# Performance work log

Measured on AMD Instinct MI355X. Metric: run time of the kernel, lower is better.

## Reference

```python
import jax, jax.numpy as jnp
import numpy as np

# --- model hyperparameters (match init_kwargs / TrajectoryDecoder defaults) ---
R, T, KREG = 3, 16, 8          # num_radii, num_theta, reg_dim
RADIUS = 40.0                  # radius_scale
VEHICLE_HIDDEN = 16
MAP_HIDDEN = 8
IN_CH = VEHICLE_HIDDEN + MAP_HIDDEN  # 24
PREDICT_WINDOW = 30
TWO_PI = 2.0 * np.pi


def _reg_roll(f):
    # f: [..., C, k] -> [..., C, k(l), k(m)] with entry f[..., c, (m-l)%k]
    m = jnp.arange(KREG)[None, :]
    l = jnp.arange(KREG)[:, None]
    return f[..., (m - l) % KREG]


def _equilinear(W, f):
    # equivariant linear map between regular reps = circular (group) conv over reg dim
    # W: [out, in, k], f: [..., in, k] -> [..., out, k]
    return jnp.einsum('oil,...ilm->...om', W, _reg_roll(f))


def _reg2rho1(f, w):
    # frequency-1 Fourier projection of the regular rep -> rho1 (2-vector); 2 free params
    ang = TWO_PI * jnp.arange(KREG) / KREG
    c, s = jnp.cos(ang), jnp.sin(ang)
    W2 = jnp.stack([w[0] * c - w[1] * s, w[0] * s + w[1] * c], axis=-1)  # [k, 2]
    return jnp.einsum('...cm,md->...cd', f, W2)


def _cts_aggregate(dst_p, src_p, H, src_mask):
    # Continuous conv aggregation: bilinear interpolation of a polar-binned kernel
    # already contracted with source features.
    # H: [B, S, R, T, O, k] per-source, per-(radius,theta)-bin transformed features
    B, S, O = src_p.shape[0], src_p.shape[1], H.shape[-2]
    rel = src_p[:, None, :, :] - dst_p[:, :, None, :]      # [B, Nd, S, 2]
    d = jnp.sqrt(jnp.sum(rel * rel, axis=-1) + 1e-12)      # [B, Nd, S]
    valid = (d < RADIUS).astype(dst_p.dtype) * src_mask[:, None, :]
    win = jnp.maximum(1.0 - (d / RADIUS) ** 2, 0.0) ** 3   # CConv window
    cnt = jnp.maximum(jnp.sum(valid, axis=-1, keepdims=True), 1.0)
    base_w = valid * win / cnt
    # radial interpolation (clamped linear)
    u = jnp.clip(d / RADIUS, 0.0, 1.0) * (R - 1)
    r0f = jnp.floor(u); wr = u - r0f
    r0 = r0f.astype(jnp.int32); r1 = jnp.minimum(r0 + 1, R - 1)
    # angular interpolation (circular linear)
    t = ((jnp.arctan2(rel[..., 1], rel[..., 0]) / TWO_PI) % 1.0) * T
    t0f = jnp.floor(t); wt = t - t0f
    t0 = t0f.astype(jnp.int32) % T; t1 = (t0 + 1) % T
    Hf = H.reshape(B, S, R * T, O, KREG)
    bidx = jnp.arange(B)[:, None, None]
    sidx = jnp.arange(S)[None, None, :]
    out = jnp.zeros((B, dst_p.shape[1], O, KREG), dtype=dst_p.dtype)
    for ri, ti, cw in ((r0, t0, (1 - wr) * (1 - wt)),
                       (r0, t1, (1 - wr) * wt),
                       (r1, t0, wr * (1 - wt)),
                       (r1, t1, wr * wt)):
        g = Hf[bidx, sidx, ri * T + ti]                    # [B, Nd, S, O, k] irregular gather
        out = out + jnp.einsum('bns,bnsok->bnok', base_w * cw, g)
    return out


def _conv_reg(K, src_p, dst_p, f, src_mask):
    # EquiCtsConv2dRegToReg: per-bin group conv over reg dim, then continuous-conv gather
    H = jnp.einsum('rtoil,bsilm->bsrtom', K, _reg_roll(f))
    return _cts_aggregate(dst_p, src_p, H, src_mask)


def _conv_rho1(K, src_p, dst_p, v, src_mask):
    # EquiCtsConv2dRho1ToReg (in_channels=1): contract 2-vector input per bin
    H = jnp.einsum('rtomd,bsd->bsrtom', K, v)
    return _cts_aggregate(dst_p, src_p, H, src_mask)


def _decode(p, feat, car_mask, K_vehicle, Wd_vehicle, K_conv1, Wd1, K_conv2, Wd2):
    out = _conv_reg(K_vehicle, p, p, feat, car_mask) + _equilinear(Wd_vehicle, feat)
    for K, Wd in ((K_conv1, Wd1), (K_conv2, Wd2)):
        inf = jax.nn.relu(out)
        oc = _conv_reg(K, p, p, inf, car_mask)
        od = _equilinear(Wd, inf)
        out = oc + od + out if od.shape[-2] == out.shape[-2] else oc + od
    return jax.nn.relu(out)


def _forward(p, feat, map_p, map_feat, car_mask, map_mask,
             K_vehicle, Wd_vehicle, K_conv1, Wd1, K_conv2, Wd2,
             Wd_back, w_rho1, K_map):
    outputs = []
    output = _decode(p, feat, car_mask, K_vehicle, Wd_vehicle, K_conv1, Wd1, K_conv2, Wd2)
    delta = _reg2rho1(output, w_rho1)                      # [B, N, 3, 2]
    outputs.append(delta.at[..., 0, :].add(p))
    for _ in range(1, PREDICT_WINDOW):
        p = p + delta[..., 0, :]
        back = jnp.tanh(_equilinear(Wd_back, output))      # [B, N, 16, k]
        feat_v = feat[..., :VEHICLE_HIDDEN, :] * back
        enc = jax.nn.relu(_conv_rho1(K_map, map_p, p, map_feat, map_mask))  # MapEncoder
        feat = jnp.concatenate([feat_v, enc], axis=-2)     # [B, N, 24, k]
        output = _decode(p, feat, car_mask, K_vehicle, Wd_vehicle, K_conv1, Wd1, K_conv2, Wd2)
        delta = _reg2rho1(output, w_rho1)
        outputs.append(delta.at[..., 0, :].add(p))
    return jnp.stack(outputs, axis=0)                      # [30, B, N, 3, 2]


def setup_inputs() -> dict:
    key = jax.random.key(0)
    ks = jax.random.split(key, 13)
    B, N, M = 8, 64, 1024
    sc = 0.1
    return {
        'p': jax.random.normal(ks[0], (B, N, 2)) * 20.0,
        'feat': jax.random.normal(ks[1], (B, N, IN_CH, KREG)),
        'map_p': jax.random.normal(ks[2], (B, M, 2)) * 20.0,
        'map_feat': jax.random.normal(ks[3], (B, M, 2)),
        'car_mask': jnp.ones((B, N), dtype=jnp.float32),
        'map_mask': jnp.ones((B, M), dtype=jnp.float32),
        'K_vehicle': jax.random.normal(ks[4], (R, T, 8, IN_CH, KREG)) * sc,
        'Wd_vehicle': jax.random.normal(ks[5], (8, IN_CH, KREG)) * sc,
        'K_conv1': jax.random.normal(ks[6], (R, T, 8, 8, KREG)) * sc,
        'Wd1': jax.random.normal(ks[7], (8, 8, KREG)) * sc,
        'K_conv2': jax.random.normal(ks[8], (R, T, 3, 8, KREG)) * sc,
        'Wd2': jax.random.normal(ks[9], (3, 8, KREG)) * sc,
        'Wd_back': jax.random.normal(ks[10], (VEHICLE_HIDDEN, 3, KREG)) * sc,
        'w_rho1': jax.random.normal(ks[11], (2,)) * sc,
        'K_map': jax.random.normal(ks[12], (R, T, MAP_HIDDEN, KREG, 2)) * sc,
    }


def reference(p, feat, map_p, map_feat, car_mask, map_mask,
              K_vehicle, Wd_vehicle, K_conv1, Wd1, K_conv2, Wd2,
              Wd_back, w_rho1, K_map):
    return _forward(p, feat, map_p, map_feat, car_mask, map_mask,
                    K_vehicle, Wd_vehicle, K_conv1, Wd1, K_conv2, Wd2,
                    Wd_back, w_rho1, K_map)
```

## Files before the change

### kernel.cpp

```cpp
#include <hip/hip_runtime.h>
#include <math.h>

#define NB 8
#define NV 64
#define NM 1024
#define NR 3
#define NT 16
#define KR 8
#define RTOT 48
#define RADIUSF 40.0f
#define TWO_PIF 6.283185307179586f

__device__ __forceinline__ void pair_geom(float relx, float rely, float mask,
                                          float& valid, float& win,
                                          int bin[4], float cw[4]) {
    float d = sqrtf(relx * relx + rely * rely + 1e-12f);
    valid = (d < RADIUSF) ? mask : 0.0f;
    float q = d * (1.0f / RADIUSF);
    float w1 = fmaxf(1.0f - q * q, 0.0f);
    win = w1 * w1 * w1;
    float u = fminf(fmaxf(q, 0.0f), 1.0f) * (float)(NR - 1);
    float r0f = floorf(u);
    float wr = u - r0f;
    int r0 = (int)r0f;
    int r1 = min(r0 + 1, NR - 1);
    float a = atan2f(rely, relx) * (1.0f / TWO_PIF);
    a = a - floorf(a);
    float t = a * (float)NT;
    float t0f = floorf(t);
    float wt = t - t0f;
    int t0 = ((int)t0f) & (NT - 1);
    int t1 = (t0 + 1) & (NT - 1);
    bin[0] = r0 * NT + t0; cw[0] = (1.0f - wr) * (1.0f - wt);
    bin[1] = r0 * NT + t1; cw[1] = (1.0f - wr) * wt;
    bin[2] = r1 * NT + t0; cw[2] = wr * (1.0f - wt);
    bin[3] = r1 * NT + t1; cw[3] = wr * wt;
}

__global__ __launch_bounds__(256) void k_trans(
        const float* __restrict__ Kv, const float* __restrict__ K1g,
        const float* __restrict__ K2g, float4* __restrict__ KTv,
        float4* __restrict__ KT1, float4* __restrict__ KT2) {
    int idx = blockIdx.x * 256 + threadIdx.x;
    if (idx < 48 * 384) {
        int j = idx / 384, p = idx % 384;
        KTv[idx] = *(const float4*)(Kv + p * 192 + j * 4);
    } else if (idx < 48 * 384 + 16 * 384) {
        int r = idx - 48 * 384;
        int j = r / 384, p = r % 384;
        KT1[r] = *(const float4*)(K1g + p * 64 + j * 4);
    } else if (idx < 48 * 384 + 16 * 384 + 16 * 144) {
        int r = idx - (48 * 384 + 16 * 384);
        int j = r / 144, p = r % 144;
        KT2[r] = *(const float4*)(K2g + p * 64 + j * 4);
    }
}

__global__ __launch_bounds__(256) void k_H0(const float* __restrict__ inb,
        const float4* __restrict__ KT, float* __restrict__ H) {
    __shared__ __align__(16) float s_f[192];
    int bs = blockIdx.x, tid = threadIdx.x;
    if (tid < 192) s_f[tid] = inb[bs * 192 + tid];
    __syncthreads();
    for (int p = tid; p < 384; p += 256) {
        float acc[KR];
#pragma unroll
        for (int m = 0; m < KR; ++m) acc[m] = 0.f;
#pragma unroll 8
        for (int i = 0; i < 24; ++i) {
            float4 k0 = KT[(2 * i) * 384 + p];
            float4 k1 = KT[(2 * i + 1) * 384 + p];
            float kk[8] = {k0.x, k0.y, k0.z, k0.w, k1.x, k1.y, k1.z, k1.w};
            float ff[8];
            *(float4*)&ff[0] = *(const float4*)&s_f[i * 8];
            *(float4*)&ff[4] = *(const float4*)&s_f[i * 8 + 4];
#pragma unroll
            for (int l = 0; l < KR; ++l) {
                float kl = kk[l];
#pragma unroll
                for (int m = 0; m < KR; ++m)
                    acc[m] = fmaf(kl, ff[(m - l) & 7], acc[m]);
            }
        }
        int rt = p >> 3, o = p & 7;
        float* hr = H + (size_t)(bs * RTOT + rt) * 64 + o * KR;
#pragma unroll
        for (int m = 0; m < KR; ++m) hr[m] = acc[m];
    }
}

__global__ __launch_bounds__(256) void k_A(int t,
        float* __restrict__ p, const float* __restrict__ out2buf,
        const float* __restrict__ H2, const float* __restrict__ Wd2,
        const float* __restrict__ w4, const int* __restrict__ bin4,
        float* __restrict__ feat,
        const float* __restrict__ w_rho1, const float* __restrict__ WdBack,
        const float* __restrict__ Kmap, const float* __restrict__ map_p,
        const float* __restrict__ map_feat, const float* __restrict__ map_mask,
        const float4* __restrict__ KTv, float* __restrict__ Hv,
        float* __restrict__ out) {
    __shared__ float s_w[256];
    __shared__ int   s_row[256];
    __shared__ float s_in[64];
    __shared__ __align__(16) float s_part[32 * 24];
    __shared__ float s_oD[24];
    __shared__ float s_w2[16];
    __shared__ float s_G4[4 * 96];
    __shared__ float s_G[96];
    __shared__ float s_wred[4];
    __shared__ __align__(16) float s_f2[192];

    int tid = threadIdx.x, bn = blockIdx.x, b = bn >> 6, n = bn & 63;
    float2 pold = *(const float2*)&p[bn * 2];

    s_w[tid] = w4[bn * 256 + tid];
    s_row[tid] = (b * NV + (tid >> 2)) * RTOT + bin4[bn * 256 + tid];
    if (tid < 64) s_in[tid] = out2buf[bn * 64 + tid];
    if (tid >= 224 && tid < 240) {
        int r = tid - 224, m = r >> 1, dd = r & 1;
        float ang = TWO_PIF * (float)m / (float)KR;
        float sn, cs; sincosf(ang, &sn, &cs);
        float w0 = w_rho1[0], wq = w_rho1[1];
        s_w2[r] = (dd == 0) ? (w0 * cs - wq * sn) : (w0 * sn + wq * cs);
    }
    if (tid < 96) { s_G4[tid] = 0.f; s_G4[96 + tid] = 0.f; s_G4[192 + tid] = 0.f; s_G4[288 + tid] = 0.f; }
    __syncthreads();

    {
        int w = tid >> 6, lane = tid & 63;
        int g = lane >> 3, c4 = lane & 7;
        float4 acc = make_float4(0.f, 0.f, 0.f, 0.f);
#pragma unroll
        for (int j = 0; j < 8; ++j) {
            int idx = w * 64 + j * 8 + g;
            float we = s_w[idx];
            if (c4 < 6) {
                float4 v = *(const float4*)&H2[(size_t)s_row[idx] * 24 + c4 * 4];
                acc.x = fmaf(we, v.x, acc.x);
                acc.y = fmaf(we, v.y, acc.y);
                acc.z = fmaf(we, v.z, acc.z);
                acc.w = fmaf(we, v.w, acc.w);
            }
        }
        if (c4 < 6) *(float4*)&s_part[(w * 8 + g) * 24 + c4 * 4] = acc;
    }
    __syncthreads();
    if (tid < 24) {
        float tot = 0.f;
#pragma unroll
        for (int k = 0; k < 32; ++k) tot += s_part[k * 24 + tid];
        int o = tid / KR, m = tid & 7;
#pragma unroll
        for (int i = 0; i < 8; ++i) {
            const float* Wr = Wd2 + (o * 8 + i) * KR;
#pragma unroll
            for (int l = 0; l < KR; ++l)
                tot = fmaf(Wr[l], fmaxf(s_in[i * KR + ((m - l) & 7)], 0.f), tot);
        }
        s_oD[tid] = fmaxf(tot, 0.f);
    }
    __syncthreads();

    float dx0 = 0.f, dy0 = 0.f;
#pragma unroll
    for (int m = 0; m < KR; ++m) {
        float v = s_oD[m];
        dx0 = fmaf(v, s_w2[m * 2 + 0], dx0);
        dy0 = fmaf(v, s_w2[m * 2 + 1], dy0);
    }
    if (tid < 6) {
        int c = tid >> 1, dd = tid & 1;
        float acc = 0.f;
#pragma unroll
        for (int m = 0; m < KR; ++m)
            acc = fmaf(s_oD[c * KR + m], s_w2[m * 2 + dd], acc);
        if (c == 0) acc += (dd ? pold.y : pold.x);
        out[(((t - 1) * NB + b) * NV + n) * 6 + tid] = acc;
    }
    float pdx = pold.x + dx0, pdy = pold.y + dy0;
    if (tid == 0) { p[bn * 2 + 0] = pdx; p[bn * 2 + 1] = pdy; }

    float lc = 0.f;
    float* myG = &s_G4[(tid >> 6) * 96];
#pragma unroll
    for (int j = 0; j < NM / 256; ++j) {
        int s = tid + j * 256;
        float2 mp = *(const float2*)&map_p[(b * NM + s) * 2];
        float valid, win; int bin[4]; float cw[4];
        pair_geom(mp.x - pdx, mp.y - pdy, map_mask[b * NM + s], valid, win, bin, cw);
        lc += valid;
        float ww = valid * win;
        if (ww > 0.f) {
            float2 f2 = *(const float2*)&map_feat[(b * NM + s) * 2];
#pragma unroll
            for (int q = 0; q < 4; ++q) {
                float w = ww * cw[q];
                atomicAdd(&myG[bin[q] * 2 + 0], w * f2.x);
                atomicAdd(&myG[bin[q] * 2 + 1], w * f2.y);
            }
        }
    }
#pragma unroll
    for (int off = 32; off > 0; off >>= 1) lc += __shfl_xor(lc, off);
    if ((tid & 63) == 0) s_wred[tid >> 6] = lc;
    __syncthreads();
    if (tid < 96) s_G[tid] = s_G4[tid] + s_G4[96 + tid] + s_G4[192 + tid] + s_G4[288 + tid];
    __syncthreads();
    float invc = 1.0f / fmaxf(s_wred[0] + s_wred[1] + s_wred[2] + s_wred[3], 1.0f);

    if (tid < 64) {
        float acc = 0.f;
#pragma unroll 8
        for (int rt = 0; rt < RTOT; ++rt) {
            float2 k2 = *(const float2*)&Kmap[(rt * 64 + tid) * 2];
            acc = fmaf(k2.x, s_G[rt * 2 + 0], acc);
            acc = fmaf(k2.y, s_G[rt * 2 + 1], acc);
        }
        s_f2[128 + tid] = fmaxf(acc * invc, 0.f);
    }
    if (tid >= 128) {
        int r = tid - 128, i = r >> 3, m = r & 7;
        float acc = 0.f;
#pragma unroll
        for (int c = 0; c < 3; ++c)
#pragma unroll
            for (int l = 0; l < KR; ++l)
                acc = fmaf(WdBack[(i * 3 + c) * 8 + l], s_oD[c * 8 + ((m - l) & 7)], acc);
        s_f2[r] = feat[bn * 192 + r] * tanhf(acc);
    }
    __syncthreads();
    if (tid < 192) feat[bn * 192 + tid] = s_f2[tid];

    for (int pp = tid; pp < 384; pp += 256) {
        float acc[KR];
#pragma unroll
        for (int m = 0; m < KR; ++m) acc[m] = 0.f;
#pragma unroll 8
        for (int i = 0; i < 24; ++i) {
            float4 k0 = KTv[(2 * i) * 384 + pp];
            float4 k1 = KTv[(2 * i + 1) * 384 + pp];
            float kk[8] = {k0.x, k0.y, k0.z, k0.w, k1.x, k1.y, k1.z, k1.w};
            float ff[8];
            *(float4*)&ff[0] = *(const float4*)&s_f2[i * 8];
            *(float4*)&ff[4] = *(const float4*)&s_f2[i * 8 + 4];
#pragma unroll
            for (int l = 0; l < KR; ++l) {
                float kl = kk[l];
#pragma unroll
                for (int m = 0; m < KR; ++m)
                    acc[m] = fmaf(kl, ff[(m - l) & 7], acc[m]);
            }
        }
        int rt = pp >> 3, o = pp & 7;
        float* hr = Hv + (size_t)(bn * RTOT + rt) * 64 + o * KR;
#pragma unroll
        for (int m = 0; m < KR; ++m) hr[m] = acc[m];
    }
}

__global__ __launch_bounds__(256) void k_B(
        const float* __restrict__ p, const float* __restrict__ car_mask,
        const float* __restrict__ feat, const float* __restrict__ Hv,
        const float* __restrict__ WdV,
        float* __restrict__ w4, int* __restrict__ bin4,
        const float4* __restrict__ KT1,
        float* __restrict__ out1, float* __restrict__ H1) {
    __shared__ float s_psrc[NV * 2];
    __shared__ float s_w[256];
    __shared__ int   s_row[256];
    __shared__ __align__(16) float s_in[192];
    __shared__ __align__(16) float s_part[16 * 64];
    __shared__ __align__(16) float s_f2[64];
    int tid = threadIdx.x, bn = blockIdx.x, b = bn >> 6, n = bn & 63;
    if (tid < 128) s_psrc[tid] = p[b * 128 + tid];
    if (tid < 192) s_in[tid] = feat[bn * 192 + tid];
    __syncthreads();
    if (tid < NV) {
        int s = tid;
        float valid, win; int bin[4]; float cw[4];
        pair_geom(s_psrc[s * 2 + 0] - s_psrc[n * 2 + 0],
                  s_psrc[s * 2 + 1] - s_psrc[n * 2 + 1],
                  car_mask[b * NV + s], valid, win, bin, cw);
        float c = valid;
#pragma unroll
        for (int off = 32; off > 0; off >>= 1) c += __shfl_xor(c, off);
        float bw = valid * win / fmaxf(c, 1.0f);
#pragma unroll
        for (int q = 0; q < 4; ++q) {
            float wv = bw * cw[q];
            s_w[s * 4 + q] = wv;
            s_row[s * 4 + q] = (b * NV + s) * RTOT + bin[q];
            w4[bn * 256 + s * 4 + q] = wv;
            bin4[bn * 256 + s * 4 + q] = bin[q];
        }
    }
    __syncthreads();
    {
        int w = tid >> 6, lane = tid & 63;
        int g = lane >> 4, c4 = lane & 15;
        float4 acc = make_float4(0.f, 0.f, 0.f, 0.f);
#pragma unroll
        for (int j = 0; j < 16; ++j) {
            int idx = w * 64 + j * 4 + g;
            float we = s_w[idx];
            float4 v = *(const float4*)&Hv[(size_t)s_row[idx] * 64 + c4 * 4];
            acc.x = fmaf(we, v.x, acc.x);
            acc.y = fmaf(we, v.y, acc.y);
            acc.z = fmaf(we, v.z, acc.z);
            acc.w = fmaf(we, v.w, acc.w);
        }
        *(float4*)&s_part[(w * 4 + g) * 64 + c4 * 4] = acc;
    }
    __syncthreads();
    if (tid < 64) {
        float tot = 0.f;
#pragma unroll
        for (int k = 0; k < 16; ++k) tot += s_part[k * 64 + tid];
        int o = tid >> 3, m = tid & 7;
#pragma unroll
        for (int i = 0; i < 24; ++i) {
            const float* Wr = WdV + (o * 24 + i) * KR;
#pragma unroll
            for (int l = 0; l < KR; ++l)
                tot = fmaf(Wr[l], s_in[i * KR + ((m - l) & 7)], tot);
        }
        out1[bn * 64 + tid] = tot;
        s_f2[tid] = fmaxf(tot, 0.f);
    }
    __syncthreads();
    for (int pp = tid; pp < 384; pp += 256) {
        float acc2[KR];
#pragma unroll
        for (int m = 0; m < KR; ++m) acc2[m] = 0.f;
#pragma unroll 4
        for (int i = 0; i < 8; ++i) {
            float4 k0 = KT1[(2 * i) * 384 + pp];
            float4 k1 = KT1[(2 * i + 1) * 384 + pp];
            float kk[8] = {k0.x, k0.y, k0.z, k0.w, k1.x, k1.y, k1.z, k1.w};
            float ff[8];
            *(float4*)&ff[0] = *(const float4*)&s_f2[i * 8];
            *(float4*)&ff[4] = *(const float4*)&s_f2[i * 8 + 4];
#pragma unroll
            for (int l = 0; l < KR; ++l) {
                float kl = kk[l];
#pragma unroll
                for (int m = 0; m < KR; ++m)
                    acc2[m] = fmaf(kl, ff[(m - l) & 7], acc2[m]);
            }
        }
        int rt = pp >> 3, o = pp & 7;
        float* hr = H1 + (size_t)(bn * RTOT + rt) * 64 + o * KR;
#pragma unroll
        for (int m = 0; m < KR; ++m) hr[m] = acc2[m];
    }
}

__global__ __launch_bounds__(256) void k_C(const float* __restrict__ out1,
        const float* __restrict__ H1, const float* __restrict__ Wd1,
        const float* __restrict__ w4, const int* __restrict__ bin4,
        const float4* __restrict__ KT2, float* __restrict__ out2,
        float* __restrict__ H2) {
    __shared__ float s_w[256];
    __shared__ int   s_row[256];
    __shared__ float s_in[64];
    __shared__ __align__(16) float s_part[16 * 64];
    __shared__ __align__(16) float s_f2[64];
    int tid = threadIdx.x, bn = blockIdx.x, b = bn >> 6;
    s_w[tid] = w4[bn * 256 + tid];
    s_row[tid] = (b * NV + (tid >> 2)) * RTOT + bin4[bn * 256 + tid];
    if (tid < 64) s_in[tid] = out1[bn * 64 + tid];
    __syncthreads();
    {
        int w = tid >> 6, lane = tid & 63;
        int g = lane >> 4, c4 = lane & 15;
        float4 acc = make_float4(0.f, 0.f, 0.f, 0.f);
#pragma unroll
        for (int j = 0; j < 16; ++j) {
            int idx = w * 64 + j * 4 + g;
            float we = s_w[idx];
            float4 v = *(const float4*)&H1[(size_t)s_row[idx] * 64 + c4 * 4];
            acc.x = fmaf(we, v.x, acc.x);
            acc.y = fmaf(we, v.y, acc.y);
            acc.z = fmaf(we, v.z, acc.z);
            acc.w = fmaf(we, v.w, acc.w);
        }
        *(float4*)&s_part[(w * 4 + g) * 64 + c4 * 4] = acc;
    }
    __syncthreads();
    if (tid < 64) {
        float tot = 0.f;
#pragma unroll
        for (int k = 0; k < 16; ++k) tot += s_part[k * 64 + tid];
        int o = tid >> 3, m = tid & 7;
#pragma unroll
        for (int i = 0; i < 8; ++i) {
            const float* Wr = Wd1 + (o * 8 + i) * KR;
#pragma unroll
            for (int l = 0; l < KR; ++l)
                tot = fmaf(Wr[l], fmaxf(s_in[i * KR + ((m - l) & 7)], 0.f), tot);
        }
        tot += s_in[tid];
        out2[bn * 64 + tid] = tot;
        s_f2[tid] = fmaxf(tot, 0.f);
    }
    __syncthreads();
    for (int pp = tid; pp < 144; pp += 256) {
        float acc2[KR];
#pragma unroll
        for (int m = 0; m < KR; ++m) acc2[m] = 0.f;
#pragma unroll 4
        for (int i = 0; i < 8; ++i) {
            float4 k0 = KT2[(2 * i) * 144 + pp];
            float4 k1 = KT2[(2 * i + 1) * 144 + pp];
            float kk[8] = {k0.x, k0.y, k0.z, k0.w, k1.x, k1.y, k1.z, k1.w};
            float ff[8];
            *(float4*)&ff[0] = *(const float4*)&s_f2[i * 8];
            *(float4*)&ff[4] = *(const float4*)&s_f2[i * 8 + 4];
#pragma unroll
            for (int l = 0; l < KR; ++l) {
                float kl = kk[l];
#pragma unroll
                for (int m = 0; m < KR; ++m)
                    acc2[m] = fmaf(kl, ff[(m - l) & 7], acc2[m]);
            }
        }
        int rt = pp / 3, o = pp - rt * 3;
        float* hr = H2 + (size_t)(bn * RTOT + rt) * 24 + o * KR;
#pragma unroll
        for (int m = 0; m < KR; ++m) hr[m] = acc2[m];
    }
}

__global__ __launch_bounds__(256) void k_fin(
        const float* __restrict__ p, const float* __restrict__ out2buf,
        const float* __restrict__ H2, const float* __restrict__ Wd2,
        const float* __restrict__ w4, const int* __restrict__ bin4,
        const float* __restrict__ w_rho1, float* __restrict__ out) {
    __shared__ float s_w[256];
    __shared__ int   s_row[256];
    __shared__ float s_in[64];
    __shared__ __align__(16) float s_part[32 * 24];
    __shared__ float s_oD[24];
    __shared__ float s_w2[16];
    int tid = threadIdx.x, bn = blockIdx.x, b = bn >> 6, n = bn & 63;
    s_w[tid] = w4[bn * 256 + tid];
    s_row[tid] = (b * NV + (tid >> 2)) * RTOT + bin4[bn * 256 + tid];
    if (tid < 64) s_in[tid] = out2buf[bn * 64 + tid];
    if (tid >= 224 && tid < 240) {
        int r = tid - 224, m = r >> 1, dd = r & 1;
        float ang = TWO_PIF * (float)m / (float)KR;
        float sn, cs; sincosf(ang, &sn, &cs);
        float w0 = w_rho1[0], wq = w_rho1[1];
        s_w2[r] = (dd == 0) ? (w0 * cs - wq * sn) : (w0 * sn + wq * cs);
    }
    __syncthreads();
    {
        int w = tid >> 6, lane = tid & 63;
        int g = lane >> 3, c4 = lane & 7;
        float4 acc = make_float4(0.f, 0.f, 0.f, 0.f);
#pragma unroll
        for (int j = 0; j < 8; ++j) {
            int idx = w * 64 + j * 8 + g;
            float we = s_w[idx];
            if (c4 < 6) {
                float4 v = *(const float4*)&H2[(size_t)s_row[idx] * 24 + c4 * 4];
                acc.x = fmaf(we, v.x, acc.x);
                acc.y = fmaf(we, v.y, acc.y);
                acc.z = fmaf(we, v.z, acc.z);
                acc.w = fmaf(we, v.w, acc.w);
            }
        }
        if (c4 < 6) *(float4*)&s_part[(w * 8 + g) * 24 + c4 * 4] = acc;
    }
    __syncthreads();
    if (tid < 24) {
        float tot = 0.f;
#pragma unroll
        for (int k = 0; k < 32; ++k) tot += s_part[k * 24 + tid];
        int o = tid / KR, m = tid & 7;
#pragma unroll
        for (int i = 0; i < 8; ++i) {
            const float* Wr = Wd2 + (o * 8 + i) * KR;
#pragma unroll
            for (int l = 0; l < KR; ++l)
                tot = fmaf(Wr[l], fmaxf(s_in[i * KR + ((m - l) & 7)], 0.f), tot);
        }
        s_oD[tid] = fmaxf(tot, 0.f);
    }
    __syncthreads();
    if (tid < 6) {
        int c = tid >> 1, dd = tid & 1;
        float acc = 0.f;
#pragma unroll
        for (int m = 0; m < KR; ++m)
            acc = fmaf(s_oD[c * KR + m], s_w2[m * 2 + dd], acc);
        if (c == 0) acc += p[bn * 2 + dd];
        out[((29 * NB + b) * NV + n) * 6 + tid] = acc;
    }
}

extern "C" void kernel_launch(void* const* d_in, const int* in_sizes, int n_in,
                              void* d_out, int out_size, void* d_ws, size_t ws_size,
                              hipStream_t stream) {
    const float* in_p     = (const float*)d_in[0];
    const float* in_feat  = (const float*)d_in[1];
    const float* map_p    = (const float*)d_in[2];
    const float* map_feat = (const float*)d_in[3];
    const float* car_mask = (const float*)d_in[4];
    const float* map_mask = (const float*)d_in[5];
    const float* Kv       = (const float*)d_in[6];
    const float* WdV      = (const float*)d_in[7];
    const float* K1       = (const float*)d_in[8];
    const float* Wd1      = (const float*)d_in[9];
    const float* K2       = (const float*)d_in[10];
    const float* Wd2      = (const float*)d_in[11];
    const float* WdBack   = (const float*)d_in[12];
    const float* w_rho1   = (const float*)d_in[13];
    const float* Kmap     = (const float*)d_in[14];

    float* ws   = (float*)d_ws;
    float* pbuf  = ws;
    float* feat  = ws + 2048;
    float* out1  = ws + 100352;
    float* out2  = ws + 133120;
    float* w4    = ws + 178176;
    int*   bin4  = (int*)(ws + 309248);
    float4* KTv  = (float4*)(ws + 440320);
    float4* KT1  = (float4*)(ws + 514048);
    float4* KT2  = (float4*)(ws + 538624);
    float* Hv    = ws + 547840;
    float* H1    = ws + 2120704;
    float* H2    = ws + 3693568;
    float* out   = (float*)d_out;

    hipMemcpyAsync(pbuf, in_p, NB * NV * 2 * sizeof(float),
                   hipMemcpyDeviceToDevice, stream);
    hipMemcpyAsync(feat, in_feat, NB * NV * 24 * KR * sizeof(float),
                   hipMemcpyDeviceToDevice, stream);

    k_trans<<<105, 256, 0, stream>>>(Kv, K1, K2, KTv, KT1, KT2);
    k_H0<<<NB * NV, 256, 0, stream>>>(feat, KTv, Hv);

    k_B<<<NB * NV, 256, 0, stream>>>(pbuf, car_mask, feat, Hv, WdV, w4, bin4, KT1, out1, H1);
    k_C<<<NB * NV, 256, 0, stream>>>(out1, H1, Wd1, w4, bin4, KT2, out2, H2);

    for (int t = 1; t < 30; ++t) {
        k_A<<<NB * NV, 256, 0, stream>>>(t, pbuf, out2, H2, Wd2, w4, bin4, feat,
                                         w_rho1, WdBack, Kmap, map_p, map_feat,
                                         map_mask, KTv, Hv, out);
        k_B<<<NB * NV, 256, 0, stream>>>(pbuf, car_mask, feat, Hv, WdV, w4, bin4, KT1, out1, H1);
        k_C<<<NB * NV, 256, 0, stream>>>(out1, H1, Wd1, w4, bin4, KT2, out2, H2);
    }
    k_fin<<<NB * NV, 256, 0, stream>>>(pbuf, out2, H2, Wd2, w4, bin4, w_rho1, out);
}
```

Baseline: 1.744 ms.

## Use polynomial atan2, privatize map histogram per lane, prefetch map data

Replaces atan2f with a minimax polynomial approximation in the pair geometry. The map-bin histogram changes from 4 per-wave shared-memory copies to 32 padded per-lane copies, which cuts atomic contention, and a 32-way reduction is added afterwards. Map positions, masks and features are loaded into registers at kernel start so their latency overlaps the earlier phases. The approximate atan2 can move points that sit near theta bin boundaries into a different bin, and the added copies raise shared-memory use and register pressure.

```diff
diff --git a/kernel.cpp b/kernel.cpp
--- a/kernel.cpp
+++ b/kernel.cpp
@@ -10,6 +10,18 @@
 #define RTOT 48
 #define RADIUSF 40.0f
 #define TWO_PIF 6.283185307179586f
+
+__device__ __forceinline__ float fast_atan2(float y, float x) {
+    float ax = fabsf(x), ay = fabsf(y);
+    float mx = fmaxf(ax, ay), mn = fminf(ax, ay);
+    float z = mn / fmaxf(mx, 1e-30f);
+    float z2 = z * z;
+    float r = fmaf(z2, fmaf(z2, fmaf(z2, fmaf(z2, 0.0208351f, -0.0851330f),
+                                     0.1801410f), -0.3302995f), 0.9998660f) * z;
+    r = (ay > ax) ? (1.57079637f - r) : r;
+    r = (x < 0.f) ? (3.14159274f - r) : r;
+    return (y < 0.f) ? -r : r;
+}
 
 __device__ __forceinline__ void pair_geom(float relx, float rely, float mask,
                                           float& valid, float& win,
@@ -24,7 +36,7 @@
     float wr = u - r0f;
     int r0 = (int)r0f;
     int r1 = min(r0 + 1, NR - 1);
-    float a = atan2f(rely, relx) * (1.0f / TWO_PIF);
+    float a = fast_atan2(rely, relx) * (1.0f / TWO_PIF);
     a = a - floorf(a);
     float t = a * (float)NT;
     float t0f = floorf(t);
@@ -105,13 +117,22 @@
     __shared__ __align__(16) float s_part[32 * 24];
     __shared__ float s_oD[24];
     __shared__ float s_w2[16];
-    __shared__ float s_G4[4 * 96];
+    __shared__ float s_G32[32 * 97];
     __shared__ float s_G[96];
     __shared__ float s_wred[4];
     __shared__ __align__(16) float s_f2[192];
 
     int tid = threadIdx.x, bn = blockIdx.x, b = bn >> 6, n = bn & 63;
     float2 pold = *(const float2*)&p[bn * 2];
+
+    float2 mp[4], mf[4]; float mm[4];
+#pragma unroll
+    for (int j = 0; j < 4; ++j) {
+        int s = tid + j * 256;
+        mp[j] = *(const float2*)&map_p[(b * NM + s) * 2];
+        mm[j] = map_mask[b * NM + s];
+        mf[j] = *(const float2*)&map_feat[(b * NM + s) * 2];
+    }
 
     s_w[tid] = w4[bn * 256 + tid];
     s_row[tid] = (b * NV + (tid >> 2)) * RTOT + bin4[bn * 256 + tid];
@@ -123,7 +144,7 @@
         float w0 = w_rho1[0], wq = w_rho1[1];
         s_w2[r] = (dd == 0) ? (w0 * cs - wq * sn) : (w0 * sn + wq * cs);
     }
-    if (tid < 96) { s_G4[tid] = 0.f; s_G4[96 + tid] = 0.f; s_G4[192 + tid] = 0.f; s_G4[288 + tid] = 0.f; }
+    for (int i = tid; i < 32 * 97; i += 256) s_G32[i] = 0.f;
     __syncthreads();
 
     {
@@ -181,22 +202,19 @@
     if (tid == 0) { p[bn * 2 + 0] = pdx; p[bn * 2 + 1] = pdy; }
 
     float lc = 0.f;
-    float* myG = &s_G4[(tid >> 6) * 96];
-#pragma unroll
-    for (int j = 0; j < NM / 256; ++j) {
-        int s = tid + j * 256;
-        float2 mp = *(const float2*)&map_p[(b * NM + s) * 2];
+    float* myG = &s_G32[(tid & 31) * 97];
+#pragma unroll
+    for (int j = 0; j < 4; ++j) {
         float valid, win; int bin[4]; float cw[4];
-        pair_geom(mp.x - pdx, mp.y - pdy, map_mask[b * NM + s], valid, win, bin, cw);
+        pair_geom(mp[j].x - pdx, mp[j].y - pdy, mm[j], valid, win, bin, cw);
         lc += valid;
         float ww = valid * win;
         if (ww > 0.f) {
-            float2 f2 = *(const float2*)&map_feat[(b * NM + s) * 2];
 #pragma unroll
             for (int q = 0; q < 4; ++q) {
                 float w = ww * cw[q];
-                atomicAdd(&myG[bin[q] * 2 + 0], w * f2.x);
-                atomicAdd(&myG[bin[q] * 2 + 1], w * f2.y);
+                atomicAdd(&myG[bin[q] * 2 + 0], w * mf[j].x);
+                atomicAdd(&myG[bin[q] * 2 + 1], w * mf[j].y);
             }
         }
     }
@@ -204,7 +222,12 @@
     for (int off = 32; off > 0; off >>= 1) lc += __shfl_xor(lc, off);
     if ((tid & 63) == 0) s_wred[tid >> 6] = lc;
     __syncthreads();
-    if (tid < 96) s_G[tid] = s_G4[tid] + s_G4[96 + tid] + s_G4[192 + tid] + s_G4[288 + tid];
+    if (tid < 96) {
+        float g = 0.f;
+#pragma unroll
+        for (int c = 0; c < 32; ++c) g += s_G32[c * 97 + tid];
+        s_G[tid] = g;
+    }
     __syncthreads();
     float invc = 1.0f / fmaxf(s_wred[0] + s_wred[1] + s_wred[2] + s_wred[3], 1.0f);
 
```

New measurement: 1.769 ms. No clear change (+1.4%).
